# Kernel optimization log

Measured on AMD Instinct MI355X. Metric: run time of the kernel, lower is better.

## Reference

```python
import jax, jax.numpy as jnp
import numpy as np

# ---- static config (matches init_kwargs) ----
IN_DIM = 1024
HIDDEN = 4096
U_OUT = 4
PROJ = HIDDEN // U_OUT          # 1024
BS = 64                          # block_size
NB = IN_DIM // BS                # 16 blocks (in == mid == out padded dims)
NRE = 3                          # n_reuploads
RANK = 64
EPS = 1e-5

# fixed stride permutation: arange.view(NB,BS).t().reshape(-1); mid_dim == in_padded so no pad/repeat
PERM = np.arange(NB * BS).reshape(NB, BS).T.reshape(-1)  # [1024]


def setup_inputs() -> dict:
    key = jax.random.key(0)
    ks = jax.random.split(key, 12)
    x = jax.random.normal(ks[0], (4, 2048, IN_DIM), dtype=jnp.float32)
    R = jax.random.normal(ks[1], (NB, BS, BS), dtype=jnp.float32) / jnp.sqrt(BS * 1.0)
    L = jax.random.normal(ks[2], (NB, BS, BS), dtype=jnp.float32) / jnp.sqrt(BS * 1.0)
    bias = jnp.zeros((PROJ,), jnp.float32)
    gamma = jnp.ones((PROJ,), jnp.float32)
    beta = jnp.zeros((PROJ,), jnp.float32)
    Wd = jax.random.normal(ks[3], (PROJ, RANK), dtype=jnp.float32) * 0.01   # down: dim->rank
    Wu = jax.random.normal(ks[4], (RANK, PROJ), dtype=jnp.float32) * 0.01   # up: rank->dim (torch init=0; nonzero for grad coverage)
    thetas = jnp.ones((NRE, PROJ), jnp.float32) + 0.1 * jax.random.normal(ks[5], (NRE, PROJ), dtype=jnp.float32)
    phis = 0.1 * jax.random.normal(ks[6], (NRE, PROJ), dtype=jnp.float32)
    Wp = jax.random.normal(ks[7], (U_OUT, 2 * NRE), dtype=jnp.float32) / jnp.sqrt(2.0 * NRE)
    bp = jnp.zeros((U_OUT,), jnp.float32)
    return {"x": x, "R": R, "L": L, "bias": bias, "gamma": gamma, "beta": beta,
            "Wd": Wd, "Wu": Wu, "thetas": thetas, "phis": phis, "Wp": Wp, "bp": bp}


def reference(x, R, L, bias, gamma, beta, Wd, Wu, thetas, phis, Wp, bp):
    B, S, _ = x.shape
    N = B * S
    # ---- MonarchProj: block-diag R, stride permute, block-diag L ----
    h = x.reshape(N, NB, BS)
    h = jnp.einsum('nbi,bij->nbj', h, R).reshape(N, NB * BS)
    h = h[:, PERM].reshape(N, NB, BS)
    h = jnp.einsum('nbi,bij->nbj', h, L).reshape(N, NB * BS)
    h = (h + bias).reshape(B, S, PROJ)
    # ---- LayerNorm ----
    mu = h.mean(-1, keepdims=True)
    var = ((h - mu) ** 2).mean(-1, keepdims=True)
    h = (h - mu) * jax.lax.rsqrt(var + EPS) * gamma + beta
    # ---- low-rank entangle: x + up(down(x)) ----
    h = h + (h @ Wd) @ Wu
    # ---- per-reupload rotation, interleaved sin/cos stacked on last dim ----
    rot = h[..., None] * thetas.T + phis.T                    # [B,S,PROJ,NRE]
    sc = jnp.stack([jnp.sin(rot), jnp.cos(rot)], axis=-1)     # [B,S,PROJ,NRE,2]
    sc = sc.reshape(B, S, PROJ, 2 * NRE)                      # [s0,c0,s1,c1,s2,c2]
    # ---- tiny final Linear then flatten ----
    out = sc @ Wp.T + bp                                      # [B,S,PROJ,U_OUT]
    return out.reshape(B, S, HIDDEN)
```

## Files before the change

kernel.cpp:

```cpp
#include <hip/hip_runtime.h>


typedef __attribute__((ext_vector_type(8))) short bf16x8;
typedef __attribute__((ext_vector_type(4))) float f32x4;

#define PITCH 1032
#define DPITCH 68
#define DHALF (16 * DPITCH)
#define SMEM_BYTES 75904

__device__ __forceinline__ unsigned short f2bf(float f) {
    unsigned u = __float_as_uint(f);
    u = (u + 0x7FFFu + ((u >> 16) & 1u)) >> 16;
    return (unsigned short)u;
}
__device__ __forceinline__ float bf2f(unsigned short h) {
    return __uint_as_float(((unsigned)h) << 16);
}
__device__ __forceinline__ unsigned cvt_pk_bf16(float a, float b) {
    unsigned r;
    asm("v_cvt_pk_bf16_f32 %0, %1, %2" : "=v"(r) : "v"(a), "v"(b));
    return r;
}
__device__ __forceinline__ void split2(float a, float b, unsigned &H, unsigned &L) {
    H = cvt_pk_bf16(a, b);
    const float ha = __uint_as_float(H << 16);
    const float hb = __uint_as_float(H & 0xFFFF0000u);
    L = cvt_pk_bf16(a - ha, b - hb);
}
__device__ __forceinline__ f32x4 MFMA(bf16x8 a, bf16x8 b, f32x4 c) {
    return __builtin_amdgcn_mfma_f32_16x16x32_bf16(a, b, c, 0, 0, 0);
}

__global__ __launch_bounds__(256) void pack_weights(
    const float* __restrict__ R, const float* __restrict__ L,
    const float* __restrict__ Wd, const float* __restrict__ Wu,
    const float* __restrict__ gamma, const float* __restrict__ beta,
    const float* __restrict__ thetas, const float* __restrict__ phis,
    unsigned short* __restrict__ wsp)
{
    const int bx = blockIdx.x;
    const int tid = threadIdx.x;
    if (bx == 256) {
        float* bc = (float*)(wsp + (size_t)64 * 8192);
        const float INV2PI = 0.15915494309189535f;
        for (int i = tid; i < 1024; i += 256) {
            float* t = bc + 128 + i * 8;
            t[0] = gamma[i];                 t[1] = beta[i];
            t[2] = thetas[i] * INV2PI;       t[3] = thetas[1024 + i] * INV2PI;
            t[4] = thetas[2048 + i] * INV2PI;
            t[5] = phis[i] * INV2PI;         t[6] = phis[1024 + i] * INV2PI;
            t[7] = phis[2048 + i] * INV2PI;
        }
        __shared__ float red[8][64];
        const int r = tid & 63, part = tid >> 6;
        float sb = 0.f, sc = 0.f;
        for (int c = part * 256; c < part * 256 + 256; ++c) {
            const float w = Wd[(size_t)c * 64 + r];
            sb += gamma[c] * w;
            sc += beta[c] * w;
        }
        red[part][r] = sb; red[part + 4][r] = sc;
        __syncthreads();
        if (part == 0) {
            bc[r]      = red[0][r] + red[1][r] + red[2][r] + red[3][r];
            bc[64 + r] = red[4][r] + red[5][r] + red[6][r] + red[7][r];
        }
        return;
    }
    const int blk = bx >> 2;
    unsigned short* dst = wsp + (size_t)blk * 8192;
    const int slot = tid + (bx & 3) * 256;
    const int fragidx = slot >> 6;
    const int l = slot & 63;
    const int kk = fragidx >> 3;
    const int nt = (fragidx >> 1) & 3;
    const int comp = fragidx & 1;
    const int g = l >> 4, r16 = l & 15;
    const int j = nt * 16 + r16;
    bf16x8 s;
    #pragma unroll
    for (int v = 0; v < 8; ++v) {
        const int k = kk * 32 + g * 8 + v;
        float w;
        if (blk < 16)      w = R[(size_t)blk * 4096 + k * 64 + j];
        else if (blk < 32) w = L[(size_t)(blk - 16) * 4096 + k * 64 + j];
        else if (blk < 48) {
            const int kglob = (blk - 32) * 64 + k;
            w = gamma[kglob] * Wd[(size_t)kglob * 64 + j];
        } else             w = Wu[(size_t)k * 1024 + (blk - 48) * 64 + j];
        unsigned short hi = f2bf(w);
        unsigned short bits = (comp == 0) ? hi : f2bf(w - bf2f(hi));
        s[v] = (short)bits;
    }
    *(bf16x8*)(dst + fragidx * 512 + l * 8) = s;
}

__global__ __launch_bounds__(512, 4) void qrun_main(
    const float* __restrict__ x, const float* __restrict__ bias,
    const float* __restrict__ Wp, const float* __restrict__ bpv,
    const unsigned short* __restrict__ wpk, float* __restrict__ out)
{
    extern __shared__ char smem[];
    unsigned short* hiP = (unsigned short*)smem;
    unsigned short* loP = hiP + 16 * PITCH;
    float* dbuf = (float*)(loP + 16 * PITCH);
    float* lnpart = dbuf + 2 * DHALF;
    float* statsR = lnpart + 256;

    const int tid = threadIdx.x;
    const int wave = tid >> 6, lane = tid & 63;
    const int g = lane >> 4, r16 = lane & 15;
    const int grp = wave >> 2, ntw = wave & 3;
    const size_t n0 = (size_t)blockIdx.x * 16;
    const int rowA = r16 * PITCH;

    {
        const float* xb = x + n0 * 1024;
        #pragma unroll
        for (int it = 0; it < 4; ++it) {
            const int base = (it * 512 + tid) * 8;
            const int row = base >> 10, col = base & 1023;
            const float4 f0 = *(const float4*)(xb + base);
            const float4 f1 = *(const float4*)(xb + base + 4);
            unsigned H0, L0, H1, L1, H2, L2, H3, L3;
            split2(f0.x, f0.y, H0, L0);
            split2(f0.z, f0.w, H1, L1);
            split2(f1.x, f1.y, H2, L2);
            split2(f1.z, f1.w, H3, L3);
            *(uint4*)(hiP + row * PITCH + col) = make_uint4(H0, H1, H2, H3);
            *(uint4*)(loP + row * PITCH + col) = make_uint4(L0, L1, L2, L3);
        }
    }
    __syncthreads();

    f32x4 acc1[8];
    #pragma unroll
    for (int bi = 0; bi < 8; ++bi) {
        const int b = grp * 8 + bi;
        const unsigned short* wb = wpk + (size_t)b * 8192;
        bf16x8 Bh0 = *(const bf16x8*)(wb + ((0*4+ntw)*2+0)*512 + lane*8);
        bf16x8 Bl0 = *(const bf16x8*)(wb + ((0*4+ntw)*2+1)*512 + lane*8);
        bf16x8 Bh1 = *(const bf16x8*)(wb + ((1*4+ntw)*2+0)*512 + lane*8);
        bf16x8 Bl1 = *(const bf16x8*)(wb + ((1*4+ntw)*2+1)*512 + lane*8);
        const int ca = b * 64 + g * 8;
        bf16x8 Ah0 = *(const bf16x8*)(hiP + rowA + ca);
        bf16x8 Al0 = *(const bf16x8*)(loP + rowA + ca);
        bf16x8 Ah1 = *(const bf16x8*)(hiP + rowA + ca + 32);
        bf16x8 Al1 = *(const bf16x8*)(loP + rowA + ca + 32);
        f32x4 a = {0.f, 0.f, 0.f, 0.f};
        a = MFMA(Ah0, Bh0, a); a = MFMA(Ah0, Bl0, a); a = MFMA(Al0, Bh0, a);
        a = MFMA(Ah1, Bh1, a); a = MFMA(Ah1, Bl1, a); a = MFMA(Al1, Bh1, a);
        acc1[bi] = a;
    }
    __syncthreads();

    {
        const int Cw = (ntw * 4 + (r16 >> 2)) * 64 + ((r16 >> 1) & 1) * 32
                     + (((grp + 2 * (r16 & 1)) ^ (r16 >> 2)) << 3);
        #pragma unroll
        for (int v = 0; v < 4; ++v) {
            const int rowv = (g * 4 + v) * PITCH;
            unsigned h0, l0, h1, l1, h2, l2, h3, l3;
            split2(acc1[0][v], acc1[1][v], h0, l0);
            split2(acc1[2][v], acc1[3][v], h1, l1);
            split2(acc1[4][v], acc1[5][v], h2, l2);
            split2(acc1[6][v], acc1[7][v], h3, l3);
            *(uint4*)(hiP + rowv + Cw) = make_uint4(h0, h1, h2, h3);
            *(uint4*)(loP + rowv + Cw) = make_uint4(l0, l1, l2, l3);
        }
    }
    __syncthreads();

    f32x4 acc2[8];
    #pragma unroll
    for (int ci = 0; ci < 8; ++ci) {
        const int c = grp * 8 + ci;
        const unsigned short* wb = wpk + (size_t)(16 + c) * 8192;
        bf16x8 Wh0 = *(const bf16x8*)(wb + ((0*4+ntw)*2+0)*512 + lane*8);
        bf16x8 Wl0 = *(const bf16x8*)(wb + ((0*4+ntw)*2+1)*512 + lane*8);
        bf16x8 Wh1 = *(const bf16x8*)(wb + ((1*4+ntw)*2+0)*512 + lane*8);
        bf16x8 Wl1 = *(const bf16x8*)(wb + ((1*4+ntw)*2+1)*512 + lane*8);
        const int gx = ((g ^ (c & 3)) << 3);
        const int c0 = rowA + c * 64 + gx;
        bf16x8 Hh0 = *(const bf16x8*)(hiP + c0);
        bf16x8 Hl0 = *(const bf16x8*)(loP + c0);
        bf16x8 Hh1 = *(const bf16x8*)(hiP + c0 + 32);
        bf16x8 Hl1 = *(const bf16x8*)(loP + c0 + 32);
        f32x4 a = {0.f, 0.f, 0.f, 0.f};
        a = MFMA(Wh0, Hh0, a); a = MFMA(Wh0, Hl0, a); a = MFMA(Wl0, Hh0, a);
        a = MFMA(Wh1, Hh1, a); a = MFMA(Wh1, Hl1, a); a = MFMA(Wl1, Hh1, a);
        acc2[ci] = a;
    }
    __syncthreads();

    {
        float s = 0.f, s2 = 0.f;
        #pragma unroll
        for (int ci = 0; ci < 8; ++ci) {
            const int c = grp * 8 + ci;
            const int ncol = c * 64 + ntw * 16 + g * 4;
            const float4 bv = *(const float4*)(bias + ncol);
            const float f0 = acc2[ci][0] + bv.x;
            const float f1 = acc2[ci][1] + bv.y;
            const float f2 = acc2[ci][2] + bv.z;
            const float f3 = acc2[ci][3] + bv.w;
            s += f0 + f1 + f2 + f3;
            s2 += f0 * f0 + f1 * f1 + f2 * f2 + f3 * f3;
            unsigned hA, lA, hB, lB;
            split2(f0, f1, hA, lA);
            split2(f2, f3, hB, lB);
            *(uint2*)(hiP + rowA + ncol) = make_uint2(hA, hB);
            *(uint2*)(loP + rowA + ncol) = make_uint2(lA, lB);
        }
        s  += __shfl_xor(s, 16);  s  += __shfl_xor(s, 32);
        s2 += __shfl_xor(s2, 16); s2 += __shfl_xor(s2, 32);
        if (g == 0) {
            lnpart[(wave * 16 + r16) * 2]     = s;
            lnpart[(wave * 16 + r16) * 2 + 1] = s2;
        }
    }
    __syncthreads();

    if (tid < 16) {
        float s = 0.f, s2 = 0.f;
        #pragma unroll
        for (int w = 0; w < 8; ++w) {
            s  += lnpart[(w * 16 + tid) * 2];
            s2 += lnpart[(w * 16 + tid) * 2 + 1];
        }
        const float mu = s * (1.f / 1024.f);
        statsR[tid * 2]     = mu;
        statsR[tid * 2 + 1] = rsqrtf(s2 * (1.f / 1024.f) - mu * mu + 1e-5f);
    }
    {
        f32x4 accd = {0.f, 0.f, 0.f, 0.f};
        #pragma unroll
        for (int ki = 0; ki < 16; ++ki) {
            const int kq = grp * 16 + ki;
            const int kb = kq >> 1, kin = kq & 1;
            const unsigned short* wb = wpk + (size_t)(32 + kb) * 8192;
            bf16x8 Wh = *(const bf16x8*)(wb + ((kin*4+ntw)*2+0)*512 + lane*8);
            bf16x8 Hh = *(const bf16x8*)(hiP + rowA + kq * 32 + g * 8);
            accd = MFMA(Wh, Hh, accd);
        }
        *(f32x4*)(dbuf + grp * DHALF + r16 * DPITCH + ntw * 16 + g * 4) = accd;
    }
    __syncthreads();

    const float* bcf = (const float*)(wpk + (size_t)64 * 8192);
    const float muT = statsR[r16 * 2], rsT = statsR[r16 * 2 + 1];
    float muR[4], rsR[4];
    #pragma unroll
    for (int v = 0; v < 4; ++v) {
        muR[v] = statsR[(g * 4 + v) * 2];
        rsR[v] = statsR[(g * 4 + v) * 2 + 1];
    }
    bf16x8 dA[2];
    #pragma unroll
    for (int kk = 0; kk < 2; ++kk) {
        const int rb = kk * 32 + g * 8;
        const float4 B0 = *(const float4*)(bcf + rb);
        const float4 B1 = *(const float4*)(bcf + rb + 4);
        const float4 C0 = *(const float4*)(bcf + 64 + rb);
        const float4 C1 = *(const float4*)(bcf + 64 + rb + 4);
        const float Ba[8] = {B0.x,B0.y,B0.z,B0.w,B1.x,B1.y,B1.z,B1.w};
        const float Ca[8] = {C0.x,C0.y,C0.z,C0.w,C1.x,C1.y,C1.z,C1.w};
        const int di = r16 * DPITCH + rb;
        const f32x4 q0 = *(const f32x4*)(dbuf + di);
        const f32x4 q1 = *(const f32x4*)(dbuf + di + 4);
        const f32x4 p0 = *(const f32x4*)(dbuf + DHALF + di);
        const f32x4 p1 = *(const f32x4*)(dbuf + DHALF + di + 4);
        float dv[8];
        #pragma unroll
        for (int v = 0; v < 4; ++v) {
            dv[v]     = rsT * (q0[v] + p0[v]) - muT * rsT * Ba[v]     + Ca[v];
            dv[v + 4] = rsT * (q1[v] + p1[v]) - muT * rsT * Ba[v + 4] + Ca[v + 4];
        }
        const uint4 uu = make_uint4(cvt_pk_bf16(dv[0], dv[1]),
                                    cvt_pk_bf16(dv[2], dv[3]),
                                    cvt_pk_bf16(dv[4], dv[5]),
                                    cvt_pk_bf16(dv[6], dv[7]));
        dA[kk] = __builtin_bit_cast(bf16x8, uu);
    }
    float wp[24];
    #pragma unroll
    for (int k2 = 0; k2 < 24; ++k2) wp[k2] = Wp[k2];
    const float bp0 = bpv[0], bp1 = bpv[1], bp2 = bpv[2], bp3 = bpv[3];

    #pragma unroll 1
    for (int j = 0; j < 8; ++j) {
        const int ntg = wave * 8 + j;
        const int nb = ntg >> 2, ntin = ntg & 3;
        const unsigned short* wb = wpk + (size_t)(48 + nb) * 8192;
        bf16x8 Bh0 = *(const bf16x8*)(wb + ((0*4+ntin)*2+0)*512 + lane*8);
        bf16x8 Bh1 = *(const bf16x8*)(wb + ((1*4+ntin)*2+0)*512 + lane*8);
        f32x4 au = {0.f, 0.f, 0.f, 0.f};
        au = MFMA(dA[0], Bh0, au);
        au = MFMA(dA[1], Bh1, au);
        const int p = ntg * 16 + r16;
        const float4 t0 = *(const float4*)(bcf + 128 + p * 8);
        const float4 t1 = *(const float4*)(bcf + 128 + p * 8 + 4);
        const float gp = t0.x, bpp = t0.y;
        const float th0 = t0.z, th1 = t0.w, th2 = t1.x;
        const float ph0 = t1.y, ph1 = t1.z, ph2 = t1.w;
        #pragma unroll
        for (int v = 0; v < 4; ++v) {
            const int row = g * 4 + v;
            const float hraw = bf2f(hiP[row * PITCH + p]) + bf2f(loP[row * PITCH + p]);
            const float hn = (hraw - muR[v]) * rsR[v] * gp + bpp;
            const float e = au[v] + hn;
            float o0 = bp0, o1 = bp1, o2 = bp2, o3 = bp3;
            float arg, sn, cs;
            asm("v_fract_f32 %0, %1" : "=v"(arg) : "v"(fmaf(e, th0, ph0)));
            asm("v_sin_f32 %0, %1" : "=v"(sn) : "v"(arg));
            asm("v_cos_f32 %0, %1" : "=v"(cs) : "v"(arg));
            o0 = fmaf(sn, wp[0],  fmaf(cs, wp[1],  o0));
            o1 = fmaf(sn, wp[6],  fmaf(cs, wp[7],  o1));
            o2 = fmaf(sn, wp[12], fmaf(cs, wp[13], o2));
            o3 = fmaf(sn, wp[18], fmaf(cs, wp[19], o3));
            asm("v_fract_f32 %0, %1" : "=v"(arg) : "v"(fmaf(e, th1, ph1)));
            asm("v_sin_f32 %0, %1" : "=v"(sn) : "v"(arg));
            asm("v_cos_f32 %0, %1" : "=v"(cs) : "v"(arg));
            o0 = fmaf(sn, wp[2],  fmaf(cs, wp[3],  o0));
            o1 = fmaf(sn, wp[8],  fmaf(cs, wp[9],  o1));
            o2 = fmaf(sn, wp[14], fmaf(cs, wp[15], o2));
            o3 = fmaf(sn, wp[20], fmaf(cs, wp[21], o3));
            asm("v_fract_f32 %0, %1" : "=v"(arg) : "v"(fmaf(e, th2, ph2)));
            asm("v_sin_f32 %0, %1" : "=v"(sn) : "v"(arg));
            asm("v_cos_f32 %0, %1" : "=v"(cs) : "v"(arg));
            o0 = fmaf(sn, wp[4],  fmaf(cs, wp[5],  o0));
            o1 = fmaf(sn, wp[10], fmaf(cs, wp[11], o1));
            o2 = fmaf(sn, wp[16], fmaf(cs, wp[17], o2));
            o3 = fmaf(sn, wp[22], fmaf(cs, wp[23], o3));
            *(float4*)(out + ((n0 + row) * 1024 + p) * 4) = make_float4(o0, o1, o2, o3);
        }
    }
}

extern "C" void kernel_launch(void* const* d_in, const int* in_sizes, int n_in,
                              void* d_out, int out_size, void* d_ws, size_t ws_size,
                              hipStream_t stream) {
    const float* x      = (const float*)d_in[0];
    const float* R      = (const float*)d_in[1];
    const float* L      = (const float*)d_in[2];
    const float* bias   = (const float*)d_in[3];
    const float* gamma  = (const float*)d_in[4];
    const float* beta   = (const float*)d_in[5];
    const float* Wd     = (const float*)d_in[6];
    const float* Wu     = (const float*)d_in[7];
    const float* thetas = (const float*)d_in[8];
    const float* phis   = (const float*)d_in[9];
    const float* Wp     = (const float*)d_in[10];
    const float* bp     = (const float*)d_in[11];
    float* out = (float*)d_out;
    unsigned short* wsp = (unsigned short*)d_ws;
    const int N = in_sizes[0] / 1024;

    (void)hipFuncSetAttribute((const void*)qrun_main,
                              hipFuncAttributeMaxDynamicSharedMemorySize, SMEM_BYTES);
    pack_weights<<<dim3(257), dim3(256), 0, stream>>>(R, L, Wd, Wu, gamma, beta,
                                                      thetas, phis, wsp);
    qrun_main<<<dim3(N / 16), dim3(512), SMEM_BYTES, stream>>>(
        x, bias, Wp, bp, wsp, out);
}
```

Before: 61.25 us.

## Split fused kernel into LN/down-proj stage and rotation/output stage via workspace

```diff
diff --git a/kernel.cpp b/kernel.cpp
--- a/kernel.cpp
+++ b/kernel.cpp
@@ -96,10 +96,11 @@
     *(bf16x8*)(dst + fragidx * 512 + l * 8) = s;
 }
 
-__global__ __launch_bounds__(512, 4) void qrun_main(
+__global__ __launch_bounds__(512, 4) void qrun_k1(
     const float* __restrict__ x, const float* __restrict__ bias,
-    const float* __restrict__ Wp, const float* __restrict__ bpv,
-    const unsigned short* __restrict__ wpk, float* __restrict__ out)
+    const float* __restrict__ gamma, const float* __restrict__ beta,
+    const unsigned short* __restrict__ wpk,
+    unsigned* __restrict__ hn, unsigned short* __restrict__ dAg)
 {
     extern __shared__ char smem[];
     unsigned short* hiP = (unsigned short*)smem;
@@ -249,43 +250,93 @@
     __syncthreads();
 
     const float* bcf = (const float*)(wpk + (size_t)64 * 8192);
-    const float muT = statsR[r16 * 2], rsT = statsR[r16 * 2 + 1];
-    float muR[4], rsR[4];
-    #pragma unroll
-    for (int v = 0; v < 4; ++v) {
-        muR[v] = statsR[(g * 4 + v) * 2];
-        rsR[v] = statsR[(g * 4 + v) * 2 + 1];
-    }
-    bf16x8 dA[2];
-    #pragma unroll
-    for (int kk = 0; kk < 2; ++kk) {
-        const int rb = kk * 32 + g * 8;
-        const float4 B0 = *(const float4*)(bcf + rb);
-        const float4 B1 = *(const float4*)(bcf + rb + 4);
-        const float4 C0 = *(const float4*)(bcf + 64 + rb);
-        const float4 C1 = *(const float4*)(bcf + 64 + rb + 4);
-        const float Ba[8] = {B0.x,B0.y,B0.z,B0.w,B1.x,B1.y,B1.z,B1.w};
-        const float Ca[8] = {C0.x,C0.y,C0.z,C0.w,C1.x,C1.y,C1.z,C1.w};
-        const int di = r16 * DPITCH + rb;
-        const f32x4 q0 = *(const f32x4*)(dbuf + di);
-        const f32x4 q1 = *(const f32x4*)(dbuf + di + 4);
-        const f32x4 p0 = *(const f32x4*)(dbuf + DHALF + di);
-        const f32x4 p1 = *(const f32x4*)(dbuf + DHALF + di + 4);
-        float dv[8];
-        #pragma unroll
-        for (int v = 0; v < 4; ++v) {
-            dv[v]     = rsT * (q0[v] + p0[v]) - muT * rsT * Ba[v]     + Ca[v];
-            dv[v + 4] = rsT * (q1[v] + p1[v]) - muT * rsT * Ba[v + 4] + Ca[v + 4];
-        }
-        const uint4 uu = make_uint4(cvt_pk_bf16(dv[0], dv[1]),
-                                    cvt_pk_bf16(dv[2], dv[3]),
-                                    cvt_pk_bf16(dv[4], dv[5]),
-                                    cvt_pk_bf16(dv[6], dv[7]));
-        dA[kk] = __builtin_bit_cast(bf16x8, uu);
-    }
+    {
+        const float muT = statsR[r16 * 2], rsT = statsR[r16 * 2 + 1];
+        #pragma unroll
+        for (int kk = 0; kk < 2; ++kk) {
+            const int rb = kk * 32 + g * 8;
+            const float4 B0 = *(const float4*)(bcf + rb);
+            const float4 B1 = *(const float4*)(bcf + rb + 4);
+            const float4 C0 = *(const float4*)(bcf + 64 + rb);
+            const float4 C1 = *(const float4*)(bcf + 64 + rb + 4);
+            const float Ba[8] = {B0.x,B0.y,B0.z,B0.w,B1.x,B1.y,B1.z,B1.w};
+            const float Ca[8] = {C0.x,C0.y,C0.z,C0.w,C1.x,C1.y,C1.z,C1.w};
+            const int di = r16 * DPITCH + rb;
+            const f32x4 q0 = *(const f32x4*)(dbuf + di);
+            const f32x4 q1 = *(const f32x4*)(dbuf + di + 4);
+            const f32x4 p0 = *(const f32x4*)(dbuf + DHALF + di);
+            const f32x4 p1 = *(const f32x4*)(dbuf + DHALF + di + 4);
+            float dv[8];
+            #pragma unroll
+            for (int v = 0; v < 4; ++v) {
+                dv[v]     = rsT * (q0[v] + p0[v]) - muT * rsT * Ba[v]     + Ca[v];
+                dv[v + 4] = rsT * (q1[v] + p1[v]) - muT * rsT * Ba[v + 4] + Ca[v + 4];
+            }
+            if (wave == 0) {
+                const uint4 uu = make_uint4(cvt_pk_bf16(dv[0], dv[1]),
+                                            cvt_pk_bf16(dv[2], dv[3]),
+                                            cvt_pk_bf16(dv[4], dv[5]),
+                                            cvt_pk_bf16(dv[6], dv[7]));
+                *(uint4*)(dAg + (size_t)blockIdx.x * 1024 + kk * 512 + lane * 8) = uu;
+            }
+        }
+    }
+
+    {
+        const int row = tid >> 5;
+        const int cb = (tid & 31) * 32;
+        const float mu = statsR[row * 2], rs = statsR[row * 2 + 1];
+        unsigned* hrow = hn + (size_t)(n0 + row) * 1024 + cb;
+        #pragma unroll
+        for (int it = 0; it < 4; ++it) {
+            const int col = cb + it * 8;
+            bf16x8 hv = *(bf16x8*)(hiP + row * PITCH + col);
+            bf16x8 lv = *(bf16x8*)(loP + row * PITCH + col);
+            const float4 gm0 = *(const float4*)(gamma + col);
+            const float4 gm1 = *(const float4*)(gamma + col + 4);
+            const float4 bt0 = *(const float4*)(beta + col);
+            const float4 bt1 = *(const float4*)(beta + col + 4);
+            const float gm[8] = {gm0.x,gm0.y,gm0.z,gm0.w,gm1.x,gm1.y,gm1.z,gm1.w};
+            const float bt[8] = {bt0.x,bt0.y,bt0.z,bt0.w,bt1.x,bt1.y,bt1.z,bt1.w};
+            float f[8];
+            #pragma unroll
+            for (int v = 0; v < 8; ++v) {
+                const float hr = bf2f((unsigned short)hv[v]) + bf2f((unsigned short)lv[v]);
+                f[v] = (hr - mu) * rs * gm[v] + bt[v];
+            }
+            unsigned u[8];
+            #pragma unroll
+            for (int pr = 0; pr < 4; ++pr) {
+                unsigned H, Lo;
+                split2(f[pr * 2], f[pr * 2 + 1], H, Lo);
+                u[pr * 2]     = (H & 0xFFFFu) | (Lo << 16);
+                u[pr * 2 + 1] = (H >> 16) | (Lo & 0xFFFF0000u);
+            }
+            *(uint4*)(hrow + it * 8)     = make_uint4(u[0], u[1], u[2], u[3]);
+            *(uint4*)(hrow + it * 8 + 4) = make_uint4(u[4], u[5], u[6], u[7]);
+        }
+    }
+}
+
+__global__ __launch_bounds__(512) void qrun_k2(
+    const unsigned short* __restrict__ wpk,
+    const unsigned* __restrict__ hn,
+    const unsigned short* __restrict__ dAg,
+    const float* __restrict__ Wp, const float* __restrict__ bpv,
+    float* __restrict__ out)
+{
+    const int tid = threadIdx.x;
+    const int wave = tid >> 6, lane = tid & 63;
+    const int g = lane >> 4, r16 = lane & 15;
+    const size_t n0 = (size_t)blockIdx.x * 16;
+
+    const bf16x8 dA0 = *(const bf16x8*)(dAg + (size_t)blockIdx.x * 1024 + lane * 8);
+    const bf16x8 dA1 = *(const bf16x8*)(dAg + (size_t)blockIdx.x * 1024 + 512 + lane * 8);
+    const float* bcf = (const float*)(wpk + (size_t)64 * 8192);
+
     float wp[24];
     #pragma unroll
-    for (int k2 = 0; k2 < 24; ++k2) wp[k2] = Wp[k2];
+    for (int k2i = 0; k2i < 24; ++k2i) wp[k2i] = Wp[k2i];
     const float bp0 = bpv[0], bp1 = bpv[1], bp2 = bpv[2], bp3 = bpv[3];
 
     #pragma unroll 1
@@ -296,20 +347,23 @@
         bf16x8 Bh0 = *(const bf16x8*)(wb + ((0*4+ntin)*2+0)*512 + lane*8);
         bf16x8 Bh1 = *(const bf16x8*)(wb + ((1*4+ntin)*2+0)*512 + lane*8);
         f32x4 au = {0.f, 0.f, 0.f, 0.f};
-        au = MFMA(dA[0], Bh0, au);
-        au = MFMA(dA[1], Bh1, au);
+        au = MFMA(dA0, Bh0, au);
+        au = MFMA(dA1, Bh1, au);
         const int p = ntg * 16 + r16;
         const float4 t0 = *(const float4*)(bcf + 128 + p * 8);
         const float4 t1 = *(const float4*)(bcf + 128 + p * 8 + 4);
-        const float gp = t0.x, bpp = t0.y;
         const float th0 = t0.z, th1 = t0.w, th2 = t1.x;
         const float ph0 = t1.y, ph1 = t1.z, ph2 = t1.w;
+        unsigned hu[4];
+        #pragma unroll
+        for (int v = 0; v < 4; ++v)
+            hu[v] = hn[(n0 + g * 4 + v) * 1024 + p];
         #pragma unroll
         for (int v = 0; v < 4; ++v) {
             const int row = g * 4 + v;
-            const float hraw = bf2f(hiP[row * PITCH + p]) + bf2f(loP[row * PITCH + p]);
-            const float hn = (hraw - muR[v]) * rsR[v] * gp + bpp;
-            const float e = au[v] + hn;
+            const float hnv = __uint_as_float(hu[v] << 16)
+                            + __uint_as_float(hu[v] & 0xFFFF0000u);
+            const float e = au[v] + hnv;
             float o0 = bp0, o1 = bp1, o2 = bp2, o3 = bp3;
             float arg, sn, cs;
             asm("v_fract_f32 %0, %1" : "=v"(arg) : "v"(fmaf(e, th0, ph0)));
@@ -357,10 +411,15 @@
     unsigned short* wsp = (unsigned short*)d_ws;
     const int N = in_sizes[0] / 1024;
 
-    (void)hipFuncSetAttribute((const void*)qrun_main,
+    unsigned* hnb        = (unsigned*)((char*)d_ws + ((size_t)2 << 20));
+    unsigned short* dAb  = (unsigned short*)((char*)d_ws + ((size_t)40 << 20));
+
+    (void)hipFuncSetAttribute((const void*)qrun_k1,
                               hipFuncAttributeMaxDynamicSharedMemorySize, SMEM_BYTES);
     pack_weights<<<dim3(257), dim3(256), 0, stream>>>(R, L, Wd, Wu, gamma, beta,
                                                       thetas, phis, wsp);
-    qrun_main<<<dim3(N / 16), dim3(512), SMEM_BYTES, stream>>>(
-        x, bias, Wp, bp, wsp, out);
-}
+    qrun_k1<<<dim3(N / 16), dim3(512), SMEM_BYTES, stream>>>(
+        x, bias, gamma, beta, wsp, hnb, dAb);
+    qrun_k2<<<dim3(N / 16), dim3(512), 0, stream>>>(
+        wsp, hnb, dAb, Wp, bp, out);
+}
```

Result: slower. 86.25 us (+40.8%).

## Process two row tiles per 1024-thread block and overlap epilogue with next tile's GEMMs

Applied to the files above, without the earlier changes.

```diff
diff --git a/kernel.cpp b/kernel.cpp
--- a/kernel.cpp
+++ b/kernel.cpp
@@ -6,8 +6,8 @@
 
 #define PITCH 1032
 #define DPITCH 68
-#define DHALF (16 * DPITCH)
-#define SMEM_BYTES 75904
+#define DQ (16 * DPITCH)
+#define SMEM_BYTES 151808
 
 __device__ __forceinline__ unsigned short f2bf(float f) {
     unsigned u = __float_as_uint(f);
@@ -96,109 +96,113 @@
     *(bf16x8*)(dst + fragidx * 512 + l * 8) = s;
 }
 
-__global__ __launch_bounds__(512, 4) void qrun_main(
+__global__ __launch_bounds__(1024, 1) void qrun_main(
     const float* __restrict__ x, const float* __restrict__ bias,
     const float* __restrict__ Wp, const float* __restrict__ bpv,
     const unsigned short* __restrict__ wpk, float* __restrict__ out)
 {
     extern __shared__ char smem[];
-    unsigned short* hiP = (unsigned short*)smem;
-    unsigned short* loP = hiP + 16 * PITCH;
-    float* dbuf = (float*)(loP + 16 * PITCH);
-    float* lnpart = dbuf + 2 * DHALF;
-    float* statsR = lnpart + 256;
+    unsigned short* hiP0 = (unsigned short*)smem;
+    unsigned short* loP0 = hiP0 + 16 * PITCH;
+    unsigned short* hiP1 = loP0 + 16 * PITCH;
+    unsigned short* loP1 = hiP1 + 16 * PITCH;
+    float* dbuf    = (float*)(loP1 + 16 * PITCH);
+    float* lnpart  = dbuf + 4 * DQ;
+    float* statsR0 = lnpart + 512;
+    float* statsR1 = statsR0 + 32;
 
     const int tid = threadIdx.x;
     const int wave = tid >> 6, lane = tid & 63;
     const int g = lane >> 4, r16 = lane & 15;
-    const int grp = wave >> 2, ntw = wave & 3;
-    const size_t n0 = (size_t)blockIdx.x * 16;
+    const int grp4 = wave >> 2, ntw = wave & 3;
     const int rowA = r16 * PITCH;
-
-    {
-        const float* xb = x + n0 * 1024;
-        #pragma unroll
-        for (int it = 0; it < 4; ++it) {
-            const int base = (it * 512 + tid) * 8;
+    const float* bcf = (const float*)(wpk + (size_t)64 * 8192);
+    const size_t t0 = (size_t)blockIdx.x * 32;
+    const size_t t1 = t0 + 16;
+
+    float wp[24];
+    #pragma unroll
+    for (int k2 = 0; k2 < 24; ++k2) wp[k2] = Wp[k2];
+    const float bp0 = bpv[0], bp1 = bpv[1], bp2 = bpv[2], bp3 = bpv[3];
+
+    auto LOADX = [&](const float* xb, unsigned short* hiP, unsigned short* loP) {
+        #pragma unroll
+        for (int it = 0; it < 2; ++it) {
+            const int base = (it * 1024 + tid) * 8;
             const int row = base >> 10, col = base & 1023;
             const float4 f0 = *(const float4*)(xb + base);
             const float4 f1 = *(const float4*)(xb + base + 4);
             unsigned H0, L0, H1, L1, H2, L2, H3, L3;
-            split2(f0.x, f0.y, H0, L0);
-            split2(f0.z, f0.w, H1, L1);
-            split2(f1.x, f1.y, H2, L2);
-            split2(f1.z, f1.w, H3, L3);
+            split2(f0.x, f0.y, H0, L0); split2(f0.z, f0.w, H1, L1);
+            split2(f1.x, f1.y, H2, L2); split2(f1.z, f1.w, H3, L3);
             *(uint4*)(hiP + row * PITCH + col) = make_uint4(H0, H1, H2, H3);
             *(uint4*)(loP + row * PITCH + col) = make_uint4(L0, L1, L2, L3);
         }
-    }
-    __syncthreads();
-
-    f32x4 acc1[8];
-    #pragma unroll
-    for (int bi = 0; bi < 8; ++bi) {
-        const int b = grp * 8 + bi;
-        const unsigned short* wb = wpk + (size_t)b * 8192;
-        bf16x8 Bh0 = *(const bf16x8*)(wb + ((0*4+ntw)*2+0)*512 + lane*8);
-        bf16x8 Bl0 = *(const bf16x8*)(wb + ((0*4+ntw)*2+1)*512 + lane*8);
-        bf16x8 Bh1 = *(const bf16x8*)(wb + ((1*4+ntw)*2+0)*512 + lane*8);
-        bf16x8 Bl1 = *(const bf16x8*)(wb + ((1*4+ntw)*2+1)*512 + lane*8);
-        const int ca = b * 64 + g * 8;
-        bf16x8 Ah0 = *(const bf16x8*)(hiP + rowA + ca);
-        bf16x8 Al0 = *(const bf16x8*)(loP + rowA + ca);
-        bf16x8 Ah1 = *(const bf16x8*)(hiP + rowA + ca + 32);
-        bf16x8 Al1 = *(const bf16x8*)(loP + rowA + ca + 32);
-        f32x4 a = {0.f, 0.f, 0.f, 0.f};
-        a = MFMA(Ah0, Bh0, a); a = MFMA(Ah0, Bl0, a); a = MFMA(Al0, Bh0, a);
-        a = MFMA(Ah1, Bh1, a); a = MFMA(Ah1, Bl1, a); a = MFMA(Al1, Bh1, a);
-        acc1[bi] = a;
-    }
-    __syncthreads();
-
-    {
+    };
+
+    auto S1 = [&](unsigned short* hiP, unsigned short* loP, f32x4* acc1) {
+        #pragma unroll
+        for (int bi = 0; bi < 4; ++bi) {
+            const int b = grp4 * 4 + bi;
+            const unsigned short* wb = wpk + (size_t)b * 8192;
+            bf16x8 Bh0 = *(const bf16x8*)(wb + ((0*4+ntw)*2+0)*512 + lane*8);
+            bf16x8 Bl0 = *(const bf16x8*)(wb + ((0*4+ntw)*2+1)*512 + lane*8);
+            bf16x8 Bh1 = *(const bf16x8*)(wb + ((1*4+ntw)*2+0)*512 + lane*8);
+            bf16x8 Bl1 = *(const bf16x8*)(wb + ((1*4+ntw)*2+1)*512 + lane*8);
+            const int ca = b * 64 + g * 8;
+            bf16x8 Ah0 = *(const bf16x8*)(hiP + rowA + ca);
+            bf16x8 Al0 = *(const bf16x8*)(loP + rowA + ca);
+            bf16x8 Ah1 = *(const bf16x8*)(hiP + rowA + ca + 32);
+            bf16x8 Al1 = *(const bf16x8*)(loP + rowA + ca + 32);
+            f32x4 a = {0.f, 0.f, 0.f, 0.f};
+            a = MFMA(Ah0, Bh0, a); a = MFMA(Ah0, Bl0, a); a = MFMA(Al0, Bh0, a);
+            a = MFMA(Ah1, Bh1, a); a = MFMA(Ah1, Bl1, a); a = MFMA(Al1, Bh1, a);
+            acc1[bi] = a;
+        }
+    };
+
+    auto PW = [&](unsigned short* hiP, unsigned short* loP, const f32x4* acc1) {
         const int Cw = (ntw * 4 + (r16 >> 2)) * 64 + ((r16 >> 1) & 1) * 32
-                     + (((grp + 2 * (r16 & 1)) ^ (r16 >> 2)) << 3);
+                     + ((((grp4 >> 1) + 2 * (r16 & 1)) ^ (r16 >> 2)) << 3)
+                     + (grp4 & 1) * 4;
         #pragma unroll
         for (int v = 0; v < 4; ++v) {
             const int rowv = (g * 4 + v) * PITCH;
-            unsigned h0, l0, h1, l1, h2, l2, h3, l3;
+            unsigned h0, l0, h1, l1;
             split2(acc1[0][v], acc1[1][v], h0, l0);
             split2(acc1[2][v], acc1[3][v], h1, l1);
-            split2(acc1[4][v], acc1[5][v], h2, l2);
-            split2(acc1[6][v], acc1[7][v], h3, l3);
-            *(uint4*)(hiP + rowv + Cw) = make_uint4(h0, h1, h2, h3);
-            *(uint4*)(loP + rowv + Cw) = make_uint4(l0, l1, l2, l3);
-        }
-    }
-    __syncthreads();
-
-    f32x4 acc2[8];
-    #pragma unroll
-    for (int ci = 0; ci < 8; ++ci) {
-        const int c = grp * 8 + ci;
-        const unsigned short* wb = wpk + (size_t)(16 + c) * 8192;
-        bf16x8 Wh0 = *(const bf16x8*)(wb + ((0*4+ntw)*2+0)*512 + lane*8);
-        bf16x8 Wl0 = *(const bf16x8*)(wb + ((0*4+ntw)*2+1)*512 + lane*8);
-        bf16x8 Wh1 = *(const bf16x8*)(wb + ((1*4+ntw)*2+0)*512 + lane*8);
-        bf16x8 Wl1 = *(const bf16x8*)(wb + ((1*4+ntw)*2+1)*512 + lane*8);
-        const int gx = ((g ^ (c & 3)) << 3);
-        const int c0 = rowA + c * 64 + gx;
-        bf16x8 Hh0 = *(const bf16x8*)(hiP + c0);
-        bf16x8 Hl0 = *(const bf16x8*)(loP + c0);
-        bf16x8 Hh1 = *(const bf16x8*)(hiP + c0 + 32);
-        bf16x8 Hl1 = *(const bf16x8*)(loP + c0 + 32);
-        f32x4 a = {0.f, 0.f, 0.f, 0.f};
-        a = MFMA(Wh0, Hh0, a); a = MFMA(Wh0, Hl0, a); a = MFMA(Wl0, Hh0, a);
-        a = MFMA(Wh1, Hh1, a); a = MFMA(Wh1, Hl1, a); a = MFMA(Wl1, Hh1, a);
-        acc2[ci] = a;
-    }
-    __syncthreads();
-
-    {
+            *(uint2*)(hiP + rowv + Cw) = make_uint2(h0, h1);
+            *(uint2*)(loP + rowv + Cw) = make_uint2(l0, l1);
+        }
+    };
+
+    auto S2 = [&](unsigned short* hiP, unsigned short* loP, f32x4* acc2) {
+        #pragma unroll
+        for (int ci = 0; ci < 4; ++ci) {
+            const int c = grp4 * 4 + ci;
+            const unsigned short* wb = wpk + (size_t)(16 + c) * 8192;
+            bf16x8 Wh0 = *(const bf16x8*)(wb + ((0*4+ntw)*2+0)*512 + lane*8);
+            bf16x8 Wl0 = *(const bf16x8*)(wb + ((0*4+ntw)*2+1)*512 + lane*8);
+            bf16x8 Wh1 = *(const bf16x8*)(wb + ((1*4+ntw)*2+0)*512 + lane*8);
+            bf16x8 Wl1 = *(const bf16x8*)(wb + ((1*4+ntw)*2+1)*512 + lane*8);
+            const int gx = ((g ^ (c & 3)) << 3);
+            const int c0 = rowA + c * 64 + gx;
+            bf16x8 Hh0 = *(const bf16x8*)(hiP + c0);
+            bf16x8 Hl0 = *(const bf16x8*)(loP + c0);
+            bf16x8 Hh1 = *(const bf16x8*)(hiP + c0 + 32);
+            bf16x8 Hl1 = *(const bf16x8*)(loP + c0 + 32);
+            f32x4 a = {0.f, 0.f, 0.f, 0.f};
+            a = MFMA(Wh0, Hh0, a); a = MFMA(Wh0, Hl0, a); a = MFMA(Wl0, Hh0, a);
+            a = MFMA(Wh1, Hh1, a); a = MFMA(Wh1, Hl1, a); a = MFMA(Wl1, Hh1, a);
+            acc2[ci] = a;
+        }
+    };
+
+    auto EPI = [&](unsigned short* hiP, unsigned short* loP, const f32x4* acc2) {
         float s = 0.f, s2 = 0.f;
         #pragma unroll
-        for (int ci = 0; ci < 8; ++ci) {
-            const int c = grp * 8 + ci;
+        for (int ci = 0; ci < 4; ++ci) {
+            const int c = grp4 * 4 + ci;
             const int ncol = c * 64 + ntw * 16 + g * 4;
             const float4 bv = *(const float4*)(bias + ncol);
             const float f0 = acc2[ci][0] + bv.x;
@@ -219,78 +223,76 @@
             lnpart[(wave * 16 + r16) * 2]     = s;
             lnpart[(wave * 16 + r16) * 2 + 1] = s2;
         }
-    }
-    __syncthreads();
-
-    if (tid < 16) {
-        float s = 0.f, s2 = 0.f;
-        #pragma unroll
-        for (int w = 0; w < 8; ++w) {
-            s  += lnpart[(w * 16 + tid) * 2];
-            s2 += lnpart[(w * 16 + tid) * 2 + 1];
-        }
-        const float mu = s * (1.f / 1024.f);
-        statsR[tid * 2]     = mu;
-        statsR[tid * 2 + 1] = rsqrtf(s2 * (1.f / 1024.f) - mu * mu + 1e-5f);
-    }
-    {
+    };
+
+    auto STATS_DOWN = [&](unsigned short* hiP, float* statsR) {
+        if (tid < 16) {
+            float s = 0.f, s2 = 0.f;
+            #pragma unroll
+            for (int w = 0; w < 16; ++w) {
+                s  += lnpart[(w * 16 + tid) * 2];
+                s2 += lnpart[(w * 16 + tid) * 2 + 1];
+            }
+            const float mu = s * (1.f / 1024.f);
+            statsR[tid * 2]     = mu;
+            statsR[tid * 2 + 1] = rsqrtf(s2 * (1.f / 1024.f) - mu * mu + 1e-5f);
+        }
         f32x4 accd = {0.f, 0.f, 0.f, 0.f};
         #pragma unroll
-        for (int ki = 0; ki < 16; ++ki) {
-            const int kq = grp * 16 + ki;
+        for (int ki = 0; ki < 8; ++ki) {
+            const int kq = grp4 * 8 + ki;
             const int kb = kq >> 1, kin = kq & 1;
             const unsigned short* wb = wpk + (size_t)(32 + kb) * 8192;
             bf16x8 Wh = *(const bf16x8*)(wb + ((kin*4+ntw)*2+0)*512 + lane*8);
             bf16x8 Hh = *(const bf16x8*)(hiP + rowA + kq * 32 + g * 8);
             accd = MFMA(Wh, Hh, accd);
         }
-        *(f32x4*)(dbuf + grp * DHALF + r16 * DPITCH + ntw * 16 + g * 4) = accd;
-    }
-    __syncthreads();
-
-    const float* bcf = (const float*)(wpk + (size_t)64 * 8192);
-    const float muT = statsR[r16 * 2], rsT = statsR[r16 * 2 + 1];
-    float muR[4], rsR[4];
-    #pragma unroll
-    for (int v = 0; v < 4; ++v) {
-        muR[v] = statsR[(g * 4 + v) * 2];
-        rsR[v] = statsR[(g * 4 + v) * 2 + 1];
-    }
-    bf16x8 dA[2];
-    #pragma unroll
-    for (int kk = 0; kk < 2; ++kk) {
-        const int rb = kk * 32 + g * 8;
-        const float4 B0 = *(const float4*)(bcf + rb);
-        const float4 B1 = *(const float4*)(bcf + rb + 4);
-        const float4 C0 = *(const float4*)(bcf + 64 + rb);
-        const float4 C1 = *(const float4*)(bcf + 64 + rb + 4);
-        const float Ba[8] = {B0.x,B0.y,B0.z,B0.w,B1.x,B1.y,B1.z,B1.w};
-        const float Ca[8] = {C0.x,C0.y,C0.z,C0.w,C1.x,C1.y,C1.z,C1.w};
-        const int di = r16 * DPITCH + rb;
-        const f32x4 q0 = *(const f32x4*)(dbuf + di);
-        const f32x4 q1 = *(const f32x4*)(dbuf + di + 4);
-        const f32x4 p0 = *(const f32x4*)(dbuf + DHALF + di);
-        const f32x4 p1 = *(const f32x4*)(dbuf + DHALF + di + 4);
-        float dv[8];
+        *(f32x4*)(dbuf + (grp4 * 16 + r16) * DPITCH + ntw * 16 + g * 4) = accd;
+    };
+
+    auto FIXUP = [&](const float* statsR, bf16x8* dA, float* muR, float* rsR) {
+        const float muT = statsR[r16 * 2], rsT = statsR[r16 * 2 + 1];
         #pragma unroll
         for (int v = 0; v < 4; ++v) {
-            dv[v]     = rsT * (q0[v] + p0[v]) - muT * rsT * Ba[v]     + Ca[v];
-            dv[v + 4] = rsT * (q1[v] + p1[v]) - muT * rsT * Ba[v + 4] + Ca[v + 4];
-        }
-        const uint4 uu = make_uint4(cvt_pk_bf16(dv[0], dv[1]),
-                                    cvt_pk_bf16(dv[2], dv[3]),
-                                    cvt_pk_bf16(dv[4], dv[5]),
-                                    cvt_pk_bf16(dv[6], dv[7]));
-        dA[kk] = __builtin_bit_cast(bf16x8, uu);
-    }
-    float wp[24];
-    #pragma unroll
-    for (int k2 = 0; k2 < 24; ++k2) wp[k2] = Wp[k2];
-    const float bp0 = bpv[0], bp1 = bpv[1], bp2 = bpv[2], bp3 = bpv[3];
-
-    #pragma unroll 1
-    for (int j = 0; j < 8; ++j) {
-        const int ntg = wave * 8 + j;
+            muR[v] = statsR[(g * 4 + v) * 2];
+            rsR[v] = statsR[(g * 4 + v) * 2 + 1];
+        }
+        #pragma unroll
+        for (int kk = 0; kk < 2; ++kk) {
+            const int rb = kk * 32 + g * 8;
+            const float4 B0 = *(const float4*)(bcf + rb);
+            const float4 B1 = *(const float4*)(bcf + rb + 4);
+            const float4 C0 = *(const float4*)(bcf + 64 + rb);
+            const float4 C1 = *(const float4*)(bcf + 64 + rb + 4);
+            const float Ba[8] = {B0.x,B0.y,B0.z,B0.w,B1.x,B1.y,B1.z,B1.w};
+            const float Ca[8] = {C0.x,C0.y,C0.z,C0.w,C1.x,C1.y,C1.z,C1.w};
+            const int di = r16 * DPITCH + rb;
+            const f32x4 s0 = *(const f32x4*)(dbuf + di)
+                           + *(const f32x4*)(dbuf + DQ + di)
+                           + *(const f32x4*)(dbuf + 2 * DQ + di)
+                           + *(const f32x4*)(dbuf + 3 * DQ + di);
+            const f32x4 s1 = *(const f32x4*)(dbuf + di + 4)
+                           + *(const f32x4*)(dbuf + DQ + di + 4)
+                           + *(const f32x4*)(dbuf + 2 * DQ + di + 4)
+                           + *(const f32x4*)(dbuf + 3 * DQ + di + 4);
+            float dv[8];
+            #pragma unroll
+            for (int v = 0; v < 4; ++v) {
+                dv[v]     = rsT * s0[v] - muT * rsT * Ba[v]     + Ca[v];
+                dv[v + 4] = rsT * s1[v] - muT * rsT * Ba[v + 4] + Ca[v + 4];
+            }
+            const uint4 uu = make_uint4(cvt_pk_bf16(dv[0], dv[1]),
+                                        cvt_pk_bf16(dv[2], dv[3]),
+                                        cvt_pk_bf16(dv[4], dv[5]),
+                                        cvt_pk_bf16(dv[6], dv[7]));
+            dA[kk] = __builtin_bit_cast(bf16x8, uu);
+        }
+    };
+
+    auto P5J = [&](int j, const unsigned short* hiP, const unsigned short* loP,
+                   const bf16x8* dA, const float* muR, const float* rsR,
+                   size_t n0) {
+        const int ntg = wave * 4 + j;
         const int nb = ntg >> 2, ntin = ntg & 3;
         const unsigned short* wb = wpk + (size_t)(48 + nb) * 8192;
         bf16x8 Bh0 = *(const bf16x8*)(wb + ((0*4+ntin)*2+0)*512 + lane*8);
@@ -299,15 +301,22 @@
         au = MFMA(dA[0], Bh0, au);
         au = MFMA(dA[1], Bh1, au);
         const int p = ntg * 16 + r16;
-        const float4 t0 = *(const float4*)(bcf + 128 + p * 8);
-        const float4 t1 = *(const float4*)(bcf + 128 + p * 8 + 4);
-        const float gp = t0.x, bpp = t0.y;
-        const float th0 = t0.z, th1 = t0.w, th2 = t1.x;
-        const float ph0 = t1.y, ph1 = t1.z, ph2 = t1.w;
+        const float4 tt0 = *(const float4*)(bcf + 128 + p * 8);
+        const float4 tt1 = *(const float4*)(bcf + 128 + p * 8 + 4);
+        const float gp = tt0.x, bpp = tt0.y;
+        const float th0 = tt0.z, th1 = tt0.w, th2 = tt1.x;
+        const float ph0 = tt1.y, ph1 = tt1.z, ph2 = tt1.w;
+        unsigned short hs[4], ls[4];
         #pragma unroll
         for (int v = 0; v < 4; ++v) {
             const int row = g * 4 + v;
-            const float hraw = bf2f(hiP[row * PITCH + p]) + bf2f(loP[row * PITCH + p]);
+            hs[v] = hiP[row * PITCH + p];
+            ls[v] = loP[row * PITCH + p];
+        }
+        #pragma unroll
+        for (int v = 0; v < 4; ++v) {
+            const int row = g * 4 + v;
+            const float hraw = bf2f(hs[v]) + bf2f(ls[v]);
             const float hn = (hraw - muR[v]) * rsR[v] * gp + bpp;
             const float e = au[v] + hn;
             float o0 = bp0, o1 = bp1, o2 = bp2, o3 = bp3;
@@ -335,7 +344,36 @@
             o3 = fmaf(sn, wp[22], fmaf(cs, wp[23], o3));
             *(float4*)(out + ((n0 + row) * 1024 + p) * 4) = make_float4(o0, o1, o2, o3);
         }
-    }
+    };
+
+    f32x4 acc1[4], acc2[4];
+    bf16x8 dA0[2], dA1[2];
+    float muR0[4], rsR0[4], muR1[4], rsR1[4];
+
+    LOADX(x + t0 * 1024, hiP0, loP0);  __syncthreads();
+    S1(hiP0, loP0, acc1);              __syncthreads();
+    PW(hiP0, loP0, acc1);              __syncthreads();
+    S2(hiP0, loP0, acc2);              __syncthreads();
+    EPI(hiP0, loP0, acc2);             __syncthreads();
+    STATS_DOWN(hiP0, statsR0);
+    LOADX(x + t1 * 1024, hiP1, loP1);  __syncthreads();
+    FIXUP(statsR0, dA0, muR0, rsR0);
+
+    P5J(0, hiP0, loP0, dA0, muR0, rsR0, t0);
+    S1(hiP1, loP1, acc1);              __syncthreads();
+    P5J(1, hiP0, loP0, dA0, muR0, rsR0, t0);
+    PW(hiP1, loP1, acc1);              __syncthreads();
+    P5J(2, hiP0, loP0, dA0, muR0, rsR0, t0);
+    S2(hiP1, loP1, acc2);              __syncthreads();
+    P5J(3, hiP0, loP0, dA0, muR0, rsR0, t0);
+    EPI(hiP1, loP1, acc2);             __syncthreads();
+    STATS_DOWN(hiP1, statsR1);         __syncthreads();
+    FIXUP(statsR1, dA1, muR1, rsR1);
+
+    P5J(0, hiP1, loP1, dA1, muR1, rsR1, t1);
+    P5J(1, hiP1, loP1, dA1, muR1, rsR1, t1);
+    P5J(2, hiP1, loP1, dA1, muR1, rsR1, t1);
+    P5J(3, hiP1, loP1, dA1, muR1, rsR1, t1);
 }
 
 extern "C" void kernel_launch(void* const* d_in, const int* in_sizes, int n_in,
@@ -361,6 +399,6 @@
                               hipFuncAttributeMaxDynamicSharedMemorySize, SMEM_BYTES);
     pack_weights<<<dim3(257), dim3(256), 0, stream>>>(R, L, Wd, Wu, gamma, beta,
                                                       thetas, phis, wsp);
-    qrun_main<<<dim3(N / 16), dim3(512), SMEM_BYTES, stream>>>(
+    qrun_main<<<dim3(N / 32), dim3(1024), SMEM_BYTES, stream>>>(
         x, bias, Wp, bp, wsp, out);
 }
```

New measurement: 77.44 us. 1.26x slower.
